# Optimization experiments

Measured on AMD Instinct MI355X. Metric: run time of the kernel, lower is better.

## Reference

```python
import jax, jax.numpy as jnp
import numpy as np

S, D = 4096, 2048  # seq_len, embedding_space == qkv_dim


def setup_inputs() -> dict:
    key = jax.random.key(0)
    k1, k2, k3, k4, k5 = jax.random.split(key, 5)
    return {
        "input_embedding": jax.random.normal(k1, (S, D), dtype=jnp.float32),
        "query_embedding": jax.random.normal(k2, (S, D), dtype=jnp.float32),
        "Wq": jax.random.normal(k3, (D, D), dtype=jnp.float32) * 0.02,
        "Wk": jax.random.normal(k4, (D, D), dtype=jnp.float32) * 0.02,
        "Wv": jax.random.normal(k5, (D, D), dtype=jnp.float32) * 0.02,
        "include_mask": 0,  # False -> causal mask applied (module's inverted logic)
    }


def reference(input_embedding, query_embedding, Wq, Wk, Wv, include_mask):
    q = query_embedding @ Wq          # [S, D]
    k = input_embedding @ Wk          # [S, D]
    v = input_embedding @ Wv          # [S, D]
    scores = (q @ k.T) / 10.0         # [S, S]; module hardcodes /10, not sqrt(d)
    if not include_mask:
        # causal: -inf strictly above the diagonal (triu with offset 1)
        s = scores.shape[0]
        causal = jnp.tril(jnp.ones((s, s), dtype=bool))
        scores = jnp.where(causal, scores, -jnp.inf)
    probs = jax.nn.softmax(scores, axis=-1)
    return probs @ v                  # [S, D]
```

## Files before the change

### kernel.cpp

```cpp
#include <hip/hip_runtime.h>
#include <hip/hip_bf16.h>
#include <math.h>

typedef __bf16 bf16_t;
typedef __bf16 bf16x8 __attribute__((ext_vector_type(8)));
typedef float f32x4 __attribute__((ext_vector_type(4)));

enum { EP_BF16 = 0, EP_SCORES = 1, EP_F32 = 2, EP_F32A = 3 };

#define MEMFENCE asm volatile("" ::: "memory")
#define BARRIER() do { MEMFENCE; __builtin_amdgcn_s_barrier(); MEMFENCE; } while (0)

__device__ __forceinline__ void gload_lds16(const void* g, void* l) {
  __builtin_amdgcn_global_load_lds(
      (const __attribute__((address_space(1))) void*)g,
      (__attribute__((address_space(3))) void*)l, 16, 0, 0);
}

template <int N>
__device__ __forceinline__ void wait_vmcnt() {
  if constexpr (N == 0)      asm volatile("s_waitcnt vmcnt(0)" ::: "memory");
  else if constexpr (N == 3) asm volatile("s_waitcnt vmcnt(3)" ::: "memory");
  else if constexpr (N == 8) asm volatile("s_waitcnt vmcnt(8)" ::: "memory");
  else static_assert(N == 0, "unsupported vmcnt");
}

__device__ __forceinline__ int xcd_swz(int bid, int nwg) {
  const int q = nwg >> 3;
  return (bid & 7) * q + (bid >> 3);
}


template <int TM, bool STG, int WAITN>
__device__ __forceinline__ void do_tile(char* smem, int slot, int sslot, size_t stoff,
                                        const char* const* gbase, const int* lbase,
                                        const int* aoff, const int* boff,
                                        f32x4 (&acc)[TM][4]) {
  bf16x8 bfr[4], af[4];
  if constexpr (TM == 8) {
#pragma unroll
    for (int n = 0; n < 4; ++n) bfr[n] = *(const bf16x8*)(smem + slot + boff[n]);
#pragma unroll
    for (int m = 0; m < 4; ++m) af[m] = *(const bf16x8*)(smem + slot + aoff[m]);
    if constexpr (STG) {
      gload_lds16(gbase[0] + stoff, smem + sslot + lbase[0]);
      gload_lds16(gbase[1] + stoff, smem + sslot + lbase[1]);
    }
    BARRIER();
    asm volatile("s_waitcnt lgkmcnt(0)" ::: "memory");
    __builtin_amdgcn_sched_barrier(0);
    __builtin_amdgcn_s_setprio(1);
#pragma unroll
    for (int m = 0; m < 4; ++m)
#pragma unroll
      for (int n = 0; n < 4; ++n)
        acc[m][n] = __builtin_amdgcn_mfma_f32_16x16x32_bf16(af[m], bfr[n], acc[m][n], 0, 0, 0);
    __builtin_amdgcn_s_setprio(0);
    BARRIER();
#pragma unroll
    for (int m = 0; m < 4; ++m) af[m] = *(const bf16x8*)(smem + slot + aoff[4 + m]);
    if constexpr (STG) {
      gload_lds16(gbase[2] + stoff, smem + sslot + lbase[2]);
      gload_lds16(gbase[3] + stoff, smem + sslot + lbase[3]);
      wait_vmcnt<WAITN>();
    }
    BARRIER();
    asm volatile("s_waitcnt lgkmcnt(0)" ::: "memory");
    __builtin_amdgcn_sched_barrier(0);
    __builtin_amdgcn_s_setprio(1);
#pragma unroll
    for (int m = 0; m < 4; ++m)
#pragma unroll
      for (int n = 0; n < 4; ++n)
        acc[4 + m][n] = __builtin_amdgcn_mfma_f32_16x16x32_bf16(af[m], bfr[n], acc[4 + m][n], 0, 0, 0);
    __builtin_amdgcn_s_setprio(0);
    BARRIER();
  } else {
#pragma unroll
    for (int n = 0; n < 4; ++n) bfr[n] = *(const bf16x8*)(smem + slot + boff[n]);
#pragma unroll
    for (int m = 0; m < 4; ++m) af[m] = *(const bf16x8*)(smem + slot + aoff[m]);
    if constexpr (STG) {
      gload_lds16(gbase[0] + stoff, smem + sslot + lbase[0]);
      gload_lds16(gbase[1] + stoff, smem + sslot + lbase[1]);
      gload_lds16(gbase[2] + stoff, smem + sslot + lbase[2]);
      wait_vmcnt<WAITN>();
    }
    BARRIER();
    asm volatile("s_waitcnt lgkmcnt(0)" ::: "memory");
    __builtin_amdgcn_sched_barrier(0);
    __builtin_amdgcn_s_setprio(1);
#pragma unroll
    for (int m = 0; m < 4; ++m)
#pragma unroll
      for (int n = 0; n < 4; ++n)
        acc[m][n] = __builtin_amdgcn_mfma_f32_16x16x32_bf16(af[m], bfr[n], acc[m][n], 0, 0, 0);
    __builtin_amdgcn_s_setprio(0);
    BARRIER();
  }
}

template <int TM, int EPI>
__device__ __forceinline__ void gemm_core(
    const bf16_t* __restrict__ A, const bf16_t* __restrict__ B,
    void* __restrict__ Cout, int Nout, int kstride, int klen,
    int row0, int col0, bool causal, float scale, char* smem)
{
  constexpr int BM = TM * 32;
  constexpr int LPT_A = BM / 128;
  constexpr int LPT = LPT_A + 2;
  constexpr int ABYTES = BM * 64;
  constexpr int SLOT = (BM + 256) * 64;
  constexpr int NSLOT = (TM == 8) ? 4 : 3;
  constexpr int DEPTH = NSLOT - 1;
  constexpr int WAITN = (DEPTH - 1) * LPT;

  const int tid = threadIdx.x;
  const int w = tid >> 6, lane = tid & 63;
  const int wr = w >> 2, wc = w & 3;

  const int nt = klen >> 5;

  const char* gbase[LPT];
  int lbase[LPT];
  {
    const int sd = (tid & 3) ^ ((tid >> 3) & 3);
    const int rrow = tid >> 2;
#pragma unroll
    for (int r = 0; r < LPT; ++r) {
      const bool isA = (r < LPT_A);
      const int rr = isA ? r : (r - LPT_A);
      const int grow = (isA ? row0 : col0) + rr * 128 + rrow;
      const bf16_t* op = isA ? A : B;
      gbase[r] = (const char*)(op + (size_t)grow * kstride) + sd * 16;
      lbase[r] = (isA ? 0 : ABYTES) + rr * 8192 + w * 1024;
    }
  }

  const int fl = lane & 15;
  const int arow_off = fl * 64 + (((lane >> 4) ^ ((fl >> 1) & 3)) * 16);
  int aoff[TM], boff[4];
#pragma unroll
  for (int m = 0; m < TM; ++m) aoff[m] = (wr * (TM * 16) + m * 16) * 64 + arow_off;
#pragma unroll
  for (int n = 0; n < 4; ++n) boff[n] = ABYTES + (wc * 64 + n * 16) * 64 + arow_off;

  f32x4 acc[TM][4] = {};

  const int npro = nt < DEPTH ? nt : DEPTH;
  for (int t = 0; t < npro; ++t)
#pragma unroll
    for (int r = 0; r < LPT; ++r)
      gload_lds16(gbase[r] + (size_t)t * 64, smem + (t % NSLOT) * SLOT + lbase[r]);

  const int nmain = nt - DEPTH;
  if (nmain > 0) {
    wait_vmcnt<WAITN>();
    BARRIER();
    for (int t = 0; t < nmain; ++t)
      do_tile<TM, true, WAITN>(smem, (t % NSLOT) * SLOT, ((t + DEPTH) % NSLOT) * SLOT,
                               (size_t)(t + DEPTH) * 64, gbase, lbase, aoff, boff, acc);
  }

  wait_vmcnt<0>();
  BARRIER();
  for (int t = nmain > 0 ? nmain : 0; t < nt; ++t)
    do_tile<TM, false, 0>(smem, (t % NSLOT) * SLOT, 0, 0, gbase, lbase, aoff, boff, acc);

  const int cr = (lane >> 4) * 4;
  const int cc = lane & 15;
#pragma unroll
  for (int m = 0; m < TM; ++m) {
#pragma unroll
    for (int n = 0; n < 4; ++n) {
#pragma unroll
      for (int i = 0; i < 4; ++i) {
        const int r = row0 + wr * (TM * 16) + m * 16 + cr + i;
        const int c = col0 + wc * 64 + n * 16 + cc;
        float v = acc[m][n][i];
        if (EPI == EP_BF16) {
          ((bf16_t*)Cout)[(size_t)r * Nout + c] = (bf16_t)v;
        } else if (EPI == EP_SCORES) {
          v *= scale;
          if (causal && c > r) v = -INFINITY;
          ((float*)Cout)[(size_t)r * Nout + c] = v;
        } else if (EPI == EP_F32) {
          ((float*)Cout)[(size_t)r * Nout + c] = v;
        } else {
          atomicAdd((float*)Cout + (size_t)r * Nout + c, v);
        }
      }
    }
  }
}

__launch_bounds__(512, 2)
__global__ void qk_k(const bf16_t* __restrict__ qe16, const bf16_t* __restrict__ ie16,
                     const bf16_t* __restrict__ WqT, const bf16_t* __restrict__ WkT,
                     bf16_t* __restrict__ q16, bf16_t* __restrict__ k16) {
  extern __shared__ __align__(16) char smem[];
  int wg = xcd_swz(blockIdx.x, gridDim.x);
  const bf16_t *A, *B; bf16_t* C;
  if (wg < 128) { A = qe16; B = WqT; C = q16; }
  else          { A = ie16; B = WkT; C = k16; wg -= 128; }
  const int row0 = (wg >> 3) * 256, col0 = (wg & 7) * 256;
  gemm_core<8, EP_BF16>(A, B, C, 2048, 2048, 2048, row0, col0, false, 1.f, smem);
}

__launch_bounds__(512, 2)
__global__ void vs_k(const bf16_t* __restrict__ WvT, const bf16_t* __restrict__ ie16,
                     const bf16_t* __restrict__ q16, const bf16_t* __restrict__ k16,
                     bf16_t* __restrict__ vT16, float* __restrict__ scores,
                     const int* __restrict__ maskflag) {
  extern __shared__ __align__(16) char smem[];
  const bool causal = maskflag[0] == 0;
  const int nsc = causal ? 136 : 256;
  const int bid = blockIdx.x;
  if (bid < nsc) {
    const int sid = xcd_swz(bid, nsc);
    int r, c;
    if (causal) {
      r = (int)((sqrtf(8.f * (float)sid + 1.f) - 1.f) * 0.5f);
      while ((r + 1) * (r + 2) / 2 <= sid) ++r;
      while (r * (r + 1) / 2 > sid) --r;
      c = sid - r * (r + 1) / 2;
    } else {
      r = sid >> 4; c = sid & 15;
    }
    gemm_core<8, EP_SCORES>(q16, k16, scores, 4096, 2048, 2048,
                            r * 256, c * 256, causal, 0.1f, smem);
  } else {
    const int j = bid - nsc;
    gemm_core<4, EP_BF16>(WvT, ie16, vT16, 4096, 2048, 2048,
                          (j >> 4) * 128, (j & 15) * 256, false, 1.f, smem);
  }
}

__launch_bounds__(512, 4)
__global__ void smv_k(const bf16_t* __restrict__ WvT, const bf16_t* __restrict__ ie16,
                      bf16_t* __restrict__ vT16,
                      const float* __restrict__ scores, bf16_t* __restrict__ probs,
                      const int* __restrict__ maskflag) {
  extern __shared__ __align__(16) char smem[];
  const bool causal = maskflag[0] == 0;
  const int nv = causal ? 136 : 256;
  const int vbase = causal ? 120 : 0;
  const int bid = blockIdx.x;
  if (bid < nv) {
    const int j = vbase + bid;
    gemm_core<4, EP_BF16>(WvT, ie16, vT16, 4096, 2048, 2048,
                          (j >> 4) * 128, (j & 15) * 256, false, 1.f, smem);
    return;
  }
  const int p = bid - nv;
  if (p >= 2048) return;
  const int tid = threadIdx.x;
  const int h = tid >> 8;
  const int t = tid & 255;
  const int row = 2 * p + h;
  const int L = causal ? (row + 1) : 4096;
  const float* srow = scores + (size_t)row * 4096;
  float v[16];
  float m = -INFINITY;
#pragma unroll
  for (int j = 0; j < 16; ++j) {
    const int idx = t + j * 256;
    v[j] = (idx < L) ? srow[idx] : -INFINITY;
    m = fmaxf(m, v[j]);
  }
#pragma unroll
  for (int off = 32; off >= 1; off >>= 1) m = fmaxf(m, __shfl_xor(m, off));
  __shared__ float redm[8];
  __shared__ float reds[8];
  if ((tid & 63) == 0) redm[tid >> 6] = m;
  __syncthreads();
  m = fmaxf(fmaxf(redm[4 * h + 0], redm[4 * h + 1]),
            fmaxf(redm[4 * h + 2], redm[4 * h + 3]));
  float s = 0.f;
#pragma unroll
  for (int j = 0; j < 16; ++j) {
    v[j] = __expf(v[j] - m);
    s += v[j];
  }
#pragma unroll
  for (int off = 32; off >= 1; off >>= 1) s += __shfl_xor(s, off);
  if ((tid & 63) == 0) reds[tid >> 6] = s;
  __syncthreads();
  s = reds[4 * h + 0] + reds[4 * h + 1] + reds[4 * h + 2] + reds[4 * h + 3];
  const float inv = 1.f / s;
  bf16_t* prow = probs + (size_t)row * 4096;
#pragma unroll
  for (int j = 0; j < 16; ++j) prow[t + j * 256] = (bf16_t)(v[j] * inv);
}

__launch_bounds__(512, 4)
__global__ void pv_k(const bf16_t* __restrict__ probs, const bf16_t* __restrict__ vT16,
                     float* __restrict__ out, const int* __restrict__ maskflag) {
  extern __shared__ __align__(16) char smem[];
  const bool causal = maskflag[0] == 0;
  const int bid = blockIdx.x;
  if (causal) {
    if (bid >= 256) return;
    const int sid  = xcd_swz(bid, 256);
    const int half = sid & 1;
    const int pair = (sid >> 1) & 15;
    const int col  = sid >> 5;
    const int blo = pair, bhi = 31 - pair;
    const int Klo = 128 * (blo + 1);
    const int cut = 2112 - Klo;
    if (half == 0) {
      gemm_core<4, EP_F32>(probs, vT16, out, 2048, 4096, Klo,
                           blo * 128, col * 256, false, 1.f, smem);
      __syncthreads();
      gemm_core<4, EP_F32A>(probs, vT16, out, 2048, 4096, cut,
                            bhi * 128, col * 256, false, 1.f, smem);
    } else {
      gemm_core<4, EP_F32A>(probs + cut, vT16 + cut, out, 2048, 4096, 2112,
                            bhi * 128, col * 256, false, 1.f, smem);
    }
  } else {
    if (bid >= 512) return;
    const int sid = xcd_swz(bid, 512);
    const int t = sid >> 1;
    const int band = t & 31, col = t >> 5;
    const int k0 = (sid & 1) ? 2048 : 0;
    gemm_core<4, EP_F32A>(probs + k0, vT16 + k0, out, 2048, 4096, 2048,
                          band * 128, col * 256, false, 1.f, smem);
  }
}


__global__ void cvt_k(const float* __restrict__ qe, const float* __restrict__ ie,
                      bf16_t* __restrict__ qe16, bf16_t* __restrict__ ie16,
                      float* __restrict__ zout, long n) {
  const int y = blockIdx.y;
  long i = ((long)blockIdx.x * blockDim.x + threadIdx.x) * 8;
  const long stride = (long)gridDim.x * blockDim.x * 8;
  if (y == 2) {
    const float4 z = make_float4(0.f, 0.f, 0.f, 0.f);
    for (; i < n; i += stride) {
      *(float4*)(zout + i) = z;
      *(float4*)(zout + i + 4) = z;
    }
    return;
  }
  const float* x = y ? ie : qe;
  bf16_t* o = y ? ie16 : qe16;
  for (; i < n; i += stride) {
    const float4 a = *(const float4*)(x + i);
    const float4 b = *(const float4*)(x + i + 4);
    bf16x8 u;
    u[0] = (__bf16)a.x; u[1] = (__bf16)a.y; u[2] = (__bf16)a.z; u[3] = (__bf16)a.w;
    u[4] = (__bf16)b.x; u[5] = (__bf16)b.y; u[6] = (__bf16)b.z; u[7] = (__bf16)b.w;
    *(bf16x8*)(o + i) = u;
  }
}

__global__ void trans_k(const float* __restrict__ Wq, const float* __restrict__ Wk,
                        const float* __restrict__ Wv,
                        bf16_t* __restrict__ WqT, bf16_t* __restrict__ WkT,
                        bf16_t* __restrict__ WvT, int Dm) {
  const float* W = blockIdx.z == 0 ? Wq : (blockIdx.z == 1 ? Wk : Wv);
  bf16_t* WT = blockIdx.z == 0 ? WqT : (blockIdx.z == 1 ? WkT : WvT);
  __shared__ float tile[32][33];
  const int bx = blockIdx.x, by = blockIdx.y;
  const int tx = threadIdx.x & 31, ty = threadIdx.x >> 5;
#pragma unroll
  for (int r = ty; r < 32; r += 8)
    tile[r][tx] = W[(size_t)(by * 32 + r) * Dm + bx * 32 + tx];
  __syncthreads();
#pragma unroll
  for (int r = ty; r < 32; r += 8)
    WT[(size_t)(bx * 32 + r) * Dm + by * 32 + tx] = (bf16_t)tile[tx][r];
}

extern "C" void kernel_launch(void* const* d_in, const int* in_sizes, int n_in,
                              void* d_out, int out_size, void* d_ws, size_t ws_size,
                              hipStream_t stream) {
  const float* ie = (const float*)d_in[0];
  const float* qe = (const float*)d_in[1];
  const float* Wq = (const float*)d_in[2];
  const float* Wk = (const float*)d_in[3];
  const float* Wv = (const float*)d_in[4];
  const int* mask = (const int*)d_in[5];
  float* out = (float*)d_out;

  const int S = 4096, D = 2048;
  char* ws = (char*)d_ws;
  const size_t MB = 1u << 20;
  bf16_t* q16  = (bf16_t*)(ws + 0 * MB);
  bf16_t* k16  = (bf16_t*)(ws + 16 * MB);
  bf16_t* vT16 = (bf16_t*)(ws + 32 * MB);
  bf16_t* ie16 = (bf16_t*)(ws + 48 * MB);
  bf16_t* WvT  = (bf16_t*)(ws + 64 * MB);
  bf16_t* qe16 = (bf16_t*)(ws + 72 * MB);
  bf16_t* WqT  = (bf16_t*)(ws + 88 * MB);
  bf16_t* WkT  = (bf16_t*)(ws + 96 * MB);
  float*  scores = (float*)(ws + 72 * MB);
  bf16_t* probs  = (bf16_t*)(ws + 0 * MB);

  hipFuncSetAttribute(reinterpret_cast<const void*>(&qk_k),
                      hipFuncAttributeMaxDynamicSharedMemorySize, 131072);
  hipFuncSetAttribute(reinterpret_cast<const void*>(&vs_k),
                      hipFuncAttributeMaxDynamicSharedMemorySize, 131072);
  hipFuncSetAttribute(reinterpret_cast<const void*>(&smv_k),
                      hipFuncAttributeMaxDynamicSharedMemorySize, 73728);
  hipFuncSetAttribute(reinterpret_cast<const void*>(&pv_k),
                      hipFuncAttributeMaxDynamicSharedMemorySize, 73728);

  cvt_k<<<dim3(1024, 3), 256, 0, stream>>>(qe, ie, qe16, ie16, out, (long)S * D);
  trans_k<<<dim3(D / 32, D / 32, 3), 256, 0, stream>>>(Wq, Wk, Wv, WqT, WkT, WvT, D);

  qk_k<<<256, 512, 131072, stream>>>(qe16, ie16, WqT, WkT, q16, k16);

  vs_k<<<256, 512, 131072, stream>>>(WvT, ie16, q16, k16, vT16, scores, mask);

  smv_k<<<2304, 512, 73728, stream>>>(WvT, ie16, vT16, scores, probs, mask);

  pv_k<<<512, 512, 73728, stream>>>(probs, vT16, out, mask);
}
```

Before: 277.2 us.

## Split PV GEMM into balanced K-chunks with fixed-point integer atomic accumulation

Replaces the paired-band causal PV scheduling with a per-band split-K scheme: each 128-row band is divided into roughly equal K-chunks, giving up to 640 causal workgroups. A new double-buffered pv_core with a 32-wide K step and a smaller LDS footprint supports more concurrent blocks. Partial results are accumulated with integer atomics on values scaled by 2^24, which keeps the sum deterministic. A follow-up kernel converts the integers back to float. The cost is an extra pass over the output, heavier atomic traffic, and fixed-point rounding error or overflow risk if partial sums grow large.

```diff
diff --git a/kernel.cpp b/kernel.cpp
--- a/kernel.cpp
+++ b/kernel.cpp
@@ -192,6 +192,87 @@
       }
     }
   }
+}
+
+__device__ __forceinline__ void pv_core(
+    const bf16_t* __restrict__ A, const bf16_t* __restrict__ B,
+    int* __restrict__ Iout, int Nout, int kstride, int klen,
+    int row0, int col0, char* smem)
+{
+  constexpr int ABYTES = 128 * 64;
+  constexpr int SLOT = (128 + 256) * 64;
+  const int tid = threadIdx.x;
+  const int w = tid >> 6, lane = tid & 63;
+  const int wr = w >> 2, wc = w & 3;
+  const int nt = klen >> 5;
+
+  const char* gbase[3];
+  int lbase[3];
+  {
+    const int sd = (tid & 3) ^ ((tid >> 3) & 3);
+    const int rrow = tid >> 2;
+#pragma unroll
+    for (int r = 0; r < 3; ++r) {
+      const bool isA = (r == 0);
+      const int rr = isA ? 0 : (r - 1);
+      const int grow = (isA ? row0 : col0) + rr * 128 + rrow;
+      gbase[r] = (const char*)((isA ? A : B) + (size_t)grow * kstride) + sd * 16;
+      lbase[r] = (isA ? 0 : ABYTES) + rr * 8192 + w * 1024;
+    }
+  }
+  const int fl = lane & 15;
+  const int arow_off = fl * 64 + (((lane >> 4) ^ ((fl >> 1) & 3)) * 16);
+  int aoff[4], boff[4];
+#pragma unroll
+  for (int m = 0; m < 4; ++m) aoff[m] = (wr * 64 + m * 16) * 64 + arow_off;
+#pragma unroll
+  for (int n = 0; n < 4; ++n) boff[n] = ABYTES + (wc * 64 + n * 16) * 64 + arow_off;
+
+  f32x4 acc[4][4] = {};
+
+#pragma unroll
+  for (int r = 0; r < 3; ++r) gload_lds16(gbase[r], smem + lbase[r]);
+  wait_vmcnt<0>();
+  BARRIER();
+
+  int slot = 0;
+  for (int t = 0; t < nt; ++t) {
+    const int cur = slot * SLOT, nxt = (slot ^ 1) * SLOT;
+    if (t + 1 < nt) {
+#pragma unroll
+      for (int r = 0; r < 3; ++r)
+        gload_lds16(gbase[r] + (size_t)(t + 1) * 64, smem + nxt + lbase[r]);
+    }
+    bf16x8 bfr[4], af[4];
+#pragma unroll
+    for (int n = 0; n < 4; ++n) bfr[n] = *(const bf16x8*)(smem + cur + boff[n]);
+#pragma unroll
+    for (int m = 0; m < 4; ++m) af[m] = *(const bf16x8*)(smem + cur + aoff[m]);
+    __builtin_amdgcn_s_setprio(1);
+#pragma unroll
+    for (int m = 0; m < 4; ++m)
+#pragma unroll
+      for (int n = 0; n < 4; ++n)
+        acc[m][n] = __builtin_amdgcn_mfma_f32_16x16x32_bf16(af[m], bfr[n], acc[m][n], 0, 0, 0);
+    __builtin_amdgcn_s_setprio(0);
+    wait_vmcnt<0>();
+    BARRIER();
+    slot ^= 1;
+  }
+
+  const int cr = (lane >> 4) * 4;
+  const int cc = lane & 15;
+#pragma unroll
+  for (int m = 0; m < 4; ++m)
+#pragma unroll
+    for (int n = 0; n < 4; ++n)
+#pragma unroll
+      for (int i = 0; i < 4; ++i) {
+        const int r = row0 + wr * 64 + m * 16 + cr + i;
+        const int c = col0 + wc * 64 + n * 16 + cc;
+        atomicAdd(Iout + (size_t)r * Nout + c,
+                  __float2int_rn(acc[m][n][i] * 16777216.0f));
+      }
 }
 
 __launch_bounds__(512, 2)
@@ -295,37 +376,46 @@
 
 __launch_bounds__(512, 4)
 __global__ void pv_k(const bf16_t* __restrict__ probs, const bf16_t* __restrict__ vT16,
-                     float* __restrict__ out, const int* __restrict__ maskflag) {
+                     int* __restrict__ iout, const int* __restrict__ maskflag) {
   extern __shared__ __align__(16) char smem[];
   const bool causal = maskflag[0] == 0;
   const int bid = blockIdx.x;
+  const int col = bid & 7;
+  const int p = bid >> 3;
+  int band, t0, tiles;
   if (causal) {
-    if (bid >= 256) return;
-    const int sid  = xcd_swz(bid, 256);
-    const int half = sid & 1;
-    const int pair = (sid >> 1) & 15;
-    const int col  = sid >> 5;
-    const int blo = pair, bhi = 31 - pair;
-    const int Klo = 128 * (blo + 1);
-    const int cut = 2112 - Klo;
-    if (half == 0) {
-      gemm_core<4, EP_F32>(probs, vT16, out, 2048, 4096, Klo,
-                           blo * 128, col * 256, false, 1.f, smem);
-      __syncthreads();
-      gemm_core<4, EP_F32A>(probs, vT16, out, 2048, 4096, cut,
-                            bhi * 128, col * 256, false, 1.f, smem);
-    } else {
-      gemm_core<4, EP_F32A>(probs + cut, vT16 + cut, out, 2048, 4096, 2112,
-                            bhi * 128, col * 256, false, 1.f, smem);
-    }
+    if (p >= 80) return;
+    int b = 0, cum = 0;
+    while (cum + ((b + 8) >> 3) <= p) { cum += (b + 8) >> 3; ++b; }
+    const int sub = p - cum;
+    const int np = (b + 8) >> 3;
+    const int Tb = 4 * (b + 1);
+    const int base = Tb / np, rem = Tb % np;
+    tiles = base + (sub < rem ? 1 : 0);
+    t0 = sub * base + (sub < rem ? sub : rem);
+    band = b;
   } else {
-    if (bid >= 512) return;
-    const int sid = xcd_swz(bid, 512);
-    const int t = sid >> 1;
-    const int band = t & 31, col = t >> 5;
-    const int k0 = (sid & 1) ? 2048 : 0;
-    gemm_core<4, EP_F32A>(probs + k0, vT16 + k0, out, 2048, 4096, 2048,
-                          band * 128, col * 256, false, 1.f, smem);
+    if (p >= 128) return;
+    band = p >> 2;
+    t0 = (p & 3) * 32;
+    tiles = 32;
+  }
+  const int k0 = t0 * 32;
+  pv_core(probs + k0, vT16 + k0, iout, 2048, 4096, tiles * 32,
+          band * 128, col * 256, smem);
+}
+
+__global__ void cvtout_k(float* __restrict__ out, long n) {
+  long i = ((long)blockIdx.x * blockDim.x + threadIdx.x) * 4;
+  const long stride = (long)gridDim.x * blockDim.x * 4;
+  for (; i < n; i += stride) {
+    int4 v = *(const int4*)((const int*)out + i);
+    float4 f;
+    f.x = (float)v.x * (1.0f / 16777216.0f);
+    f.y = (float)v.y * (1.0f / 16777216.0f);
+    f.z = (float)v.z * (1.0f / 16777216.0f);
+    f.w = (float)v.w * (1.0f / 16777216.0f);
+    *(float4*)(out + i) = f;
   }
 }
 
@@ -406,7 +496,7 @@
   hipFuncSetAttribute(reinterpret_cast<const void*>(&smv_k),
                       hipFuncAttributeMaxDynamicSharedMemorySize, 73728);
   hipFuncSetAttribute(reinterpret_cast<const void*>(&pv_k),
-                      hipFuncAttributeMaxDynamicSharedMemorySize, 73728);
+                      hipFuncAttributeMaxDynamicSharedMemorySize, 49152);
 
   cvt_k<<<dim3(1024, 3), 256, 0, stream>>>(qe, ie, qe16, ie16, out, (long)S * D);
   trans_k<<<dim3(D / 32, D / 32, 3), 256, 0, stream>>>(Wq, Wk, Wv, WqT, WkT, WvT, D);
@@ -417,5 +507,7 @@
 
   smv_k<<<2304, 512, 73728, stream>>>(WvT, ie16, vT16, scores, probs, mask);
 
-  pv_k<<<512, 512, 73728, stream>>>(probs, vT16, out, mask);
-}
+  pv_k<<<1024, 512, 49152, stream>>>(probs, vT16, (int*)out, mask);
+
+  cvtout_k<<<2048, 256, 0, stream>>>(out, (long)S * D);
+}
```

Result: slower. 303.3 us (+9.4%).

## Rebalance PV split-K with fixed-point int atomics and move V projection into scores kernel

Applied to the files above, without the earlier changes.

Moves the whole V projection into the scores kernel using larger 256-row tiles, which leaves a standalone softmax kernel. PV is rewritten as a stream-K style causal decomposition: 32 equal-work chunks per column tile, each using 256x256 tiles. Partial sums are accumulated with integer atomics on values scaled by 2^24, and a new kernel converts them back to float. This is meant to remove the load imbalance of the causal triangle and make atomic accumulation deterministic. It adds an extra pass over the output, and the fixed-point format risks overflow or loss of precision.

```diff
diff --git a/kernel.cpp b/kernel.cpp
--- a/kernel.cpp
+++ b/kernel.cpp
@@ -6,7 +6,7 @@
 typedef __bf16 bf16x8 __attribute__((ext_vector_type(8)));
 typedef float f32x4 __attribute__((ext_vector_type(4)));
 
-enum { EP_BF16 = 0, EP_SCORES = 1, EP_F32 = 2, EP_F32A = 3 };
+enum { EP_BF16 = 0, EP_SCORES = 1, EP_F32 = 2, EP_F32A = 3, EP_I32A = 4 };
 
 #define MEMFENCE asm volatile("" ::: "memory")
 #define BARRIER() do { MEMFENCE; __builtin_amdgcn_s_barrier(); MEMFENCE; } while (0)
@@ -186,8 +186,11 @@
           ((float*)Cout)[(size_t)r * Nout + c] = v;
         } else if (EPI == EP_F32) {
           ((float*)Cout)[(size_t)r * Nout + c] = v;
+        } else if (EPI == EP_F32A) {
+          atomicAdd((float*)Cout + (size_t)r * Nout + c, v);
         } else {
-          atomicAdd((float*)Cout + (size_t)r * Nout + c, v);
+          atomicAdd((int*)Cout + (size_t)r * Nout + c,
+                    __float2int_rn(v * 16777216.0f));
         }
       }
     }
@@ -231,29 +234,17 @@
                             r * 256, c * 256, causal, 0.1f, smem);
   } else {
     const int j = bid - nsc;
-    gemm_core<4, EP_BF16>(WvT, ie16, vT16, 4096, 2048, 2048,
-                          (j >> 4) * 128, (j & 15) * 256, false, 1.f, smem);
+    if (j >= 128) return;
+    gemm_core<8, EP_BF16>(WvT, ie16, vT16, 4096, 2048, 2048,
+                          (j >> 4) * 256, (j & 15) * 256, false, 1.f, smem);
   }
 }
 
 __launch_bounds__(512, 4)
-__global__ void smv_k(const bf16_t* __restrict__ WvT, const bf16_t* __restrict__ ie16,
-                      bf16_t* __restrict__ vT16,
-                      const float* __restrict__ scores, bf16_t* __restrict__ probs,
-                      const int* __restrict__ maskflag) {
-  extern __shared__ __align__(16) char smem[];
+__global__ void sm_k(const float* __restrict__ scores, bf16_t* __restrict__ probs,
+                     const int* __restrict__ maskflag) {
   const bool causal = maskflag[0] == 0;
-  const int nv = causal ? 136 : 256;
-  const int vbase = causal ? 120 : 0;
-  const int bid = blockIdx.x;
-  if (bid < nv) {
-    const int j = vbase + bid;
-    gemm_core<4, EP_BF16>(WvT, ie16, vT16, 4096, 2048, 2048,
-                          (j >> 4) * 128, (j & 15) * 256, false, 1.f, smem);
-    return;
-  }
-  const int p = bid - nv;
-  if (p >= 2048) return;
+  const int p = blockIdx.x;
   const int tid = threadIdx.x;
   const int h = tid >> 8;
   const int t = tid & 255;
@@ -293,39 +284,50 @@
   for (int j = 0; j < 16; ++j) prow[t + j * 256] = (bf16_t)(v[j] * inv);
 }
 
-__launch_bounds__(512, 4)
+__launch_bounds__(512, 2)
 __global__ void pv_k(const bf16_t* __restrict__ probs, const bf16_t* __restrict__ vT16,
-                     float* __restrict__ out, const int* __restrict__ maskflag) {
+                     int* __restrict__ iout, const int* __restrict__ maskflag) {
   extern __shared__ __align__(16) char smem[];
   const bool causal = maskflag[0] == 0;
   const int bid = blockIdx.x;
+  const int col = bid & 7;
+  const int p = bid >> 3;
   if (causal) {
-    if (bid >= 256) return;
-    const int sid  = xcd_swz(bid, 256);
-    const int half = sid & 1;
-    const int pair = (sid >> 1) & 15;
-    const int col  = sid >> 5;
-    const int blo = pair, bhi = 31 - pair;
-    const int Klo = 128 * (blo + 1);
-    const int cut = 2112 - Klo;
-    if (half == 0) {
-      gemm_core<4, EP_F32>(probs, vT16, out, 2048, 4096, Klo,
-                           blo * 128, col * 256, false, 1.f, smem);
-      __syncthreads();
-      gemm_core<4, EP_F32A>(probs, vT16, out, 2048, 4096, cut,
-                            bhi * 128, col * 256, false, 1.f, smem);
-    } else {
-      gemm_core<4, EP_F32A>(probs + cut, vT16 + cut, out, 2048, 4096, 2112,
-                            bhi * 128, col * 256, false, 1.f, smem);
+    if (p >= 32) return;
+    const int t0g = p * 34, t1g = t0g + 34;
+    for (int b = 0; b < 16; ++b) {
+      const int cb = 4 * b * (b + 1);
+      const int nb = 8 * (b + 1);
+      const int s0 = max(t0g, cb), s1 = min(t1g, cb + nb);
+      if (s0 < s1) {
+        const int k0 = (s0 - cb) * 32;
+        const int klen = (s1 - s0) * 32;
+        gemm_core<8, EP_I32A>(probs + k0, vT16 + k0, iout, 2048, 4096, klen,
+                              b * 256, col * 256, false, 1.f, smem);
+        __syncthreads();
+      }
+      if (cb + nb >= t1g) break;
     }
   } else {
-    if (bid >= 512) return;
-    const int sid = xcd_swz(bid, 512);
-    const int t = sid >> 1;
-    const int band = t & 31, col = t >> 5;
-    const int k0 = (sid & 1) ? 2048 : 0;
-    gemm_core<4, EP_F32A>(probs + k0, vT16 + k0, out, 2048, 4096, 2048,
-                          band * 128, col * 256, false, 1.f, smem);
+    if (p >= 64) return;
+    const int band = p >> 2;
+    const int k0 = (p & 3) * 1024;
+    gemm_core<8, EP_I32A>(probs + k0, vT16 + k0, iout, 2048, 4096, 1024,
+                          band * 256, col * 256, false, 1.f, smem);
+  }
+}
+
+__global__ void cvtout_k(float* __restrict__ out, long n) {
+  long i = ((long)blockIdx.x * blockDim.x + threadIdx.x) * 4;
+  const long stride = (long)gridDim.x * blockDim.x * 4;
+  for (; i < n; i += stride) {
+    int4 v = *(const int4*)((const int*)out + i);
+    float4 f;
+    f.x = (float)v.x * (1.0f / 16777216.0f);
+    f.y = (float)v.y * (1.0f / 16777216.0f);
+    f.z = (float)v.z * (1.0f / 16777216.0f);
+    f.w = (float)v.w * (1.0f / 16777216.0f);
+    *(float4*)(out + i) = f;
   }
 }
 
@@ -403,19 +405,19 @@
                       hipFuncAttributeMaxDynamicSharedMemorySize, 131072);
   hipFuncSetAttribute(reinterpret_cast<const void*>(&vs_k),
                       hipFuncAttributeMaxDynamicSharedMemorySize, 131072);
-  hipFuncSetAttribute(reinterpret_cast<const void*>(&smv_k),
-                      hipFuncAttributeMaxDynamicSharedMemorySize, 73728);
   hipFuncSetAttribute(reinterpret_cast<const void*>(&pv_k),
-                      hipFuncAttributeMaxDynamicSharedMemorySize, 73728);
+                      hipFuncAttributeMaxDynamicSharedMemorySize, 131072);
 
   cvt_k<<<dim3(1024, 3), 256, 0, stream>>>(qe, ie, qe16, ie16, out, (long)S * D);
   trans_k<<<dim3(D / 32, D / 32, 3), 256, 0, stream>>>(Wq, Wk, Wv, WqT, WkT, WvT, D);
 
   qk_k<<<256, 512, 131072, stream>>>(qe16, ie16, WqT, WkT, q16, k16);
 
-  vs_k<<<256, 512, 131072, stream>>>(WvT, ie16, q16, k16, vT16, scores, mask);
-
-  smv_k<<<2304, 512, 73728, stream>>>(WvT, ie16, vT16, scores, probs, mask);
-
-  pv_k<<<512, 512, 73728, stream>>>(probs, vT16, out, mask);
-}
+  vs_k<<<384, 512, 131072, stream>>>(WvT, ie16, q16, k16, vT16, scores, mask);
+
+  sm_k<<<2048, 512, 0, stream>>>(scores, probs, mask);
+
+  pv_k<<<512, 512, 131072, stream>>>(probs, vT16, (int*)out, mask);
+
+  cvtout_k<<<2048, 256, 0, stream>>>(out, (long)S * D);
+}
```

Result: slower. 335.6 us (+21.1%).
